# Performance work log

Hardware: AMD Instinct MI355X
Metric: run time of the kernel (lower is better)

## Reference

```python
import jax, jax.numpy as jnp
import numpy as np

DIM = 1024
HEADS = 16
NUM_EXPERTS = 8
TOP_K = 2
INNER = 4 * DIM
EPS = 1e-5
NEG = -1e9


def setup_inputs() -> dict:
    key = jax.random.key(0)
    ks = jax.random.split(key, 12)
    s = 0.02
    return {
        "x": jax.random.normal(ks[0], (4, 1024, DIM), dtype=jnp.float32),
        "qkv_w": jax.random.normal(ks[1], (DIM, 3 * DIM), dtype=jnp.float32) * s,
        "out_w": jax.random.normal(ks[2], (DIM, DIM), dtype=jnp.float32) * s,
        "out_b": jnp.zeros((DIM,), dtype=jnp.float32),
        "thresh": jnp.float32(-2.0),
        "ln1_g": jnp.ones((DIM,), dtype=jnp.float32),
        "ln1_b": jnp.zeros((DIM,), dtype=jnp.float32),
        "ln2_g": jnp.ones((DIM,), dtype=jnp.float32),
        "ln2_b": jnp.zeros((DIM,), dtype=jnp.float32),
        "gate_w": jax.random.normal(ks[3], (DIM, NUM_EXPERTS), dtype=jnp.float32) * s,
        "w1": jax.random.normal(ks[4], (NUM_EXPERTS, DIM, INNER), dtype=jnp.float32) * s,
        "b1": jnp.zeros((NUM_EXPERTS, INNER), dtype=jnp.float32),
        "w2": jax.random.normal(ks[5], (NUM_EXPERTS, INNER, DIM), dtype=jnp.float32) * s,
        "b2": jnp.zeros((NUM_EXPERTS, DIM), dtype=jnp.float32),
    }


def _layernorm(x, g, b):
    mu = jnp.mean(x, axis=-1, keepdims=True)
    var = jnp.mean(jnp.square(x - mu), axis=-1, keepdims=True)
    return (x - mu) * jax.lax.rsqrt(var + EPS) * g + b


def reference(x, qkv_w, out_w, out_b, thresh, ln1_g, ln1_b, ln2_g, ln2_b,
              gate_w, w1, b1, w2, b2):
    B, N, D = x.shape
    H = HEADS
    Dh = D // H
    scale = Dh ** -0.5

    # --- Sparse attention (pre-norm, eval mode: dropout off) ---
    h = _layernorm(x, ln1_g, ln1_b)
    qkv = h @ qkv_w                                   # [B,N,3D]
    q, k, v = jnp.split(qkv, 3, axis=-1)
    def heads(t):
        return t.reshape(B, N, H, Dh).transpose(0, 2, 1, 3)  # [B,H,N,Dh]
    q, k, v = heads(q), heads(k), heads(v)
    dots = jnp.einsum("bhid,bhjd->bhij", q, k) * scale
    dots = jnp.where(dots < thresh, jnp.float32(NEG), dots)  # learnable sparsity
    attn = jax.nn.softmax(dots, axis=-1)
    o = jnp.einsum("bhij,bhjd->bhid", attn, v)
    o = o.transpose(0, 2, 1, 3).reshape(B, N, D)
    x = x + o @ out_w + out_b

    # --- MoE FFN (pre-norm) ---
    h2 = _layernorm(x, ln2_g, ln2_b).reshape(-1, D)   # [T,D]
    T = h2.shape[0]
    logits = h2 @ gate_w                              # [T,E]
    probs = jax.nn.softmax(logits, axis=-1)
    aux_loss = NUM_EXPERTS * jnp.sum(probs.mean(0) * probs.sum(0))

    top_w, top_i = jax.lax.top_k(logits, TOP_K)       # [T,k]
    top_w = jax.nn.softmax(top_w, axis=-1)
    # dense combine weights: [T,E], zero for unselected experts
    combine = jnp.zeros((T, NUM_EXPERTS), dtype=h2.dtype)
    combine = combine.at[jnp.arange(T)[:, None], top_i].set(top_w)

    out = jnp.zeros_like(h2)
    for e in range(NUM_EXPERTS):
        y = jax.nn.gelu(h2 @ w1[e] + b1[e], approximate=False) @ w2[e] + b2[e]
        out = out + combine[:, e:e + 1] * y

    x = x + out.reshape(B, N, D)
    return x, aux_loss
```

## Files before the change

kernel.cpp:

```cpp
#include <hip/hip_runtime.h>
#include <math.h>

#define DIM 1024
#define THREE_DIM 3072
#define INNER 4096
#define NTOK 4096
#define NPAIR 8192
#define NEXP 8
#define MAXMB 72
#define PARTROWS (MAXMB*128)

typedef __attribute__((ext_vector_type(8))) short bf16x8;
typedef __attribute__((ext_vector_type(4))) float f32x4;

__device__ __forceinline__ unsigned short f2bf(float f){
    unsigned int x = __float_as_uint(f);
    unsigned int r = x + 0x7fffu + ((x >> 16) & 1u);
    return (unsigned short)(r >> 16);
}

__device__ __forceinline__ unsigned short us4c(ushort4 v, int i){
    return i == 0 ? v.x : (i == 1 ? v.y : (i == 2 ? v.z : v.w));
}

__device__ __forceinline__ void glds16(const void* g, void* l){
    __builtin_amdgcn_global_load_lds(
        (const __attribute__((address_space(1))) void*)g,
        (__attribute__((address_space(3))) void*)l, 16, 0, 0);
}

__device__ __forceinline__ int xcd_swz(){
    int cpx = gridDim.x >> 3;
    return (blockIdx.x & 7) * cpx + (blockIdx.x >> 3);
}

template<int WRITE_BF>
__global__ __launch_bounds__(256)
void ln_kernel(const float* __restrict__ X, const float* __restrict__ g,
               const float* __restrict__ b, float* __restrict__ outF,
               unsigned short* __restrict__ outB)
{
    int row = blockIdx.x;
    int t = threadIdx.x;
    const float4 v = *((const float4*)(X + (size_t)row*DIM) + t);
    float s = v.x + v.y + v.z + v.w;
    #pragma unroll
    for (int m = 1; m < 64; m <<= 1) s += __shfl_xor(s, m, 64);
    __shared__ float red[8];
    int wid = t >> 6, lane = t & 63;
    if (lane == 0) red[wid] = s;
    __syncthreads();
    float mu = (red[0]+red[1]+red[2]+red[3]) * (1.0f/DIM);
    float dx = v.x-mu, dy = v.y-mu, dz = v.z-mu, dw = v.w-mu;
    float s2 = dx*dx + dy*dy + dz*dz + dw*dw;
    #pragma unroll
    for (int m = 1; m < 64; m <<= 1) s2 += __shfl_xor(s2, m, 64);
    if (lane == 0) red[4+wid] = s2;
    __syncthreads();
    float var = (red[4]+red[5]+red[6]+red[7]) * (1.0f/DIM);
    float inv = rsqrtf(var + 1e-5f);
    const float4 gg = *((const float4*)g + t);
    const float4 bb = *((const float4*)b + t);
    float y0 = dx*inv*gg.x + bb.x;
    float y1 = dy*inv*gg.y + bb.y;
    float y2 = dz*inv*gg.z + bb.z;
    float y3 = dw*inv*gg.w + bb.w;
    if (outF){
        float4 o; o.x=y0; o.y=y1; o.z=y2; o.w=y3;
        *((float4*)(outF + (size_t)row*DIM) + t) = o;
    }
    if (WRITE_BF){
        ushort4 u; u.x=f2bf(y0); u.y=f2bf(y1); u.z=f2bf(y2); u.w=f2bf(y3);
        *((ushort4*)(outB + (size_t)row*DIM) + t) = u;
    }
}

template<int MODE>
__global__ __launch_bounds__(256)
void gemm_bf(const unsigned short* __restrict__ A,
             const unsigned short* __restrict__ BT,
             int K, int N, int gnx,
             const float* __restrict__ bias, const float* __restrict__ resid,
             unsigned short* __restrict__ outB, float* __restrict__ outF)
{
    __shared__ __align__(16) unsigned short As[128*64];
    __shared__ __align__(16) unsigned short Bs[128*64];
    int fid = xcd_swz();
    int nx = fid % gnx, my = fid / gnx;
    int m0 = my * 128, n0 = nx * 128;
    int t = threadIdx.x, lane = t & 63, wid = t >> 6;
    size_t aoff[4], boff[4];
    #pragma unroll
    for (int it = 0; it < 4; ++it){
        int chunk = it*256 + wid*64 + lane;
        int r = chunk >> 3, c16 = chunk & 7;
        int c16s = c16 ^ (r & 7);
        aoff[it] = (size_t)(m0 + r)*K + (size_t)(c16s*8);
        boff[it] = (size_t)(n0 + r)*K + (size_t)(c16s*8);
    }
    int wm = wid >> 1, wn = wid & 1;
    f32x4 acc[4][4];
    #pragma unroll
    for (int mi = 0; mi < 4; ++mi)
        #pragma unroll
        for (int ni = 0; ni < 4; ++ni)
            #pragma unroll
            for (int q = 0; q < 4; ++q) acc[mi][ni][q] = 0.f;

    for (int k0 = 0; k0 < K; k0 += 64){
        __syncthreads();
        #pragma unroll
        for (int it = 0; it < 4; ++it){
            glds16(A  + aoff[it] + k0, As + (size_t)(it*256 + wid*64)*8);
            glds16(BT + boff[it] + k0, Bs + (size_t)(it*256 + wid*64)*8);
        }
        __syncthreads();
        bf16x8 af[4][2], bg[4][2];
        #pragma unroll
        for (int mi = 0; mi < 4; ++mi){
            int row = wm*64 + mi*16 + (lane & 15);
            #pragma unroll
            for (int ks = 0; ks < 2; ++ks){
                int cg = (ks*4 + (lane >> 4)) ^ (row & 7);
                af[mi][ks] = *(const bf16x8*)&As[row*64 + cg*8];
            }
        }
        #pragma unroll
        for (int ni = 0; ni < 4; ++ni){
            int row = wn*64 + ni*16 + (lane & 15);
            #pragma unroll
            for (int ks = 0; ks < 2; ++ks){
                int cg = (ks*4 + (lane >> 4)) ^ (row & 7);
                bg[ni][ks] = *(const bf16x8*)&Bs[row*64 + cg*8];
            }
        }
        #pragma unroll
        for (int ks = 0; ks < 2; ++ks)
            #pragma unroll
            for (int mi = 0; mi < 4; ++mi)
                #pragma unroll
                for (int ni = 0; ni < 4; ++ni)
                    acc[mi][ni] = __builtin_amdgcn_mfma_f32_16x16x32_bf16(
                                      af[mi][ks], bg[ni][ks], acc[mi][ni], 0, 0, 0);
    }
    #pragma unroll
    for (int mi = 0; mi < 4; ++mi){
        #pragma unroll
        for (int ni = 0; ni < 4; ++ni){
            int ccol = n0 + wn*64 + ni*16 + (lane & 15);
            #pragma unroll
            for (int j = 0; j < 4; ++j){
                int row = m0 + wm*64 + mi*16 + (lane >> 4)*4 + j;
                float v = acc[mi][ni][j];
                if (MODE == 0){
                    outB[(size_t)row*N + ccol] = f2bf(v);
                } else {
                    outF[(size_t)row*N + ccol] =
                        v + bias[ccol] + resid[(size_t)row*N + ccol];
                }
            }
        }
    }
}

__global__ __launch_bounds__(256)
void attn4_kernel(const unsigned short* __restrict__ qkv,
                  unsigned short* __restrict__ O,
                  const float* __restrict__ threshp)
{
    __shared__ __align__(16) unsigned short Qs[64*64];
    __shared__ __align__(16) unsigned short Ks[64*64];
    __shared__ __align__(16) unsigned short Vp[8*520];
    __shared__ __align__(16) unsigned short Ps[4*1024];

    int fid = xcd_swz();
    int qt = fid & 15, hh = (fid >> 4) & 15, bb = fid >> 8;
    int t = threadIdx.x, lane = t & 63, w = t >> 6;
    int arow = lane & 15, agrp = lane >> 4;
    int qrow0 = bb*1024 + qt*64;
    float thresh = threshp[0];

    #pragma unroll
    for (int it = 0; it < 2; ++it){
        int chunk = it*256 + w*64 + lane;
        int r = chunk >> 3, c16 = chunk & 7;
        glds16(qkv + (size_t)(qrow0+r)*3072 + hh*64 + ((c16 ^ (r & 7))*8),
               Qs + (size_t)(it*256 + w*64)*8);
    }
    __syncthreads();
    bf16x8 qf[2];
    {
        int row = w*16 + arow;
        #pragma unroll
        for (int s = 0; s < 2; ++s){
            int c = (s*4 + agrp) ^ (row & 7);
            qf[s] = *(const bf16x8*)&Qs[row*64 + c*8];
        }
    }

    float m_[4], l_[4];
    f32x4 acc[4];
    #pragma unroll
    for (int j = 0; j < 4; ++j){ m_[j] = -INFINITY; l_[j] = 0.f; }
    #pragma unroll
    for (int d4 = 0; d4 < 4; ++d4)
        #pragma unroll
        for (int j = 0; j < 4; ++j) acc[d4][j] = 0.f;

    for (int kt = 0; kt < 16; ++kt){
        __syncthreads();
        int krow0 = bb*1024 + kt*64;
        #pragma unroll
        for (int it = 0; it < 2; ++it){
            int chunk = it*256 + w*64 + lane;
            int r = chunk >> 3, c16 = chunk & 7;
            glds16(qkv + (size_t)(krow0+r)*3072 + 1024 + hh*64 + ((c16 ^ (r & 7))*8),
                   Ks + (size_t)(it*256 + w*64)*8);
        }
        if (t < 128){
            int jc = t & 7, d0 = (t >> 3) * 4;
            ushort4 u[8];
            #pragma unroll
            for (int jj = 0; jj < 8; ++jj)
                u[jj] = *(const ushort4*)(qkv + (size_t)(krow0 + jc*8 + jj)*3072
                                          + 2048 + hh*64 + d0);
            #pragma unroll
            for (int i = 0; i < 4; ++i){
                ushort4 a, b;
                a.x = us4c(u[0], i); a.y = us4c(u[1], i);
                a.z = us4c(u[2], i); a.w = us4c(u[3], i);
                b.x = us4c(u[4], i); b.y = us4c(u[5], i);
                b.z = us4c(u[6], i); b.w = us4c(u[7], i);
                *(ushort4*)&Vp[jc*520 + (d0+i)*8]     = a;
                *(ushort4*)&Vp[jc*520 + (d0+i)*8 + 4] = b;
            }
        }
        __syncthreads();

        f32x4 sv[4];
        #pragma unroll
        for (int n = 0; n < 4; ++n)
            #pragma unroll
            for (int j = 0; j < 4; ++j) sv[n][j] = 0.f;
        #pragma unroll
        for (int n = 0; n < 4; ++n){
            int krow = n*16 + arow;
            #pragma unroll
            for (int s = 0; s < 2; ++s){
                int c = (s*4 + agrp) ^ (krow & 7);
                bf16x8 kf = *(const bf16x8*)&Ks[krow*64 + c*8];
                sv[n] = __builtin_amdgcn_mfma_f32_16x16x32_bf16(qf[s], kf, sv[n], 0, 0, 0);
            }
        }
        #pragma unroll
        for (int n = 0; n < 4; ++n)
            #pragma unroll
            for (int j = 0; j < 4; ++j){
                float s = sv[n][j] * 0.125f;
                sv[n][j] = (s < thresh) ? -1e9f : s;
            }
        float tmax[4], fac[4], rsum[4];
        #pragma unroll
        for (int j = 0; j < 4; ++j)
            tmax[j] = fmaxf(fmaxf(sv[0][j], sv[1][j]), fmaxf(sv[2][j], sv[3][j]));
        #pragma unroll
        for (int msk = 1; msk < 16; msk <<= 1)
            #pragma unroll
            for (int j = 0; j < 4; ++j)
                tmax[j] = fmaxf(tmax[j], __shfl_xor(tmax[j], msk, 64));
        #pragma unroll
        for (int j = 0; j < 4; ++j){
            float mn = fmaxf(m_[j], tmax[j]);
            fac[j] = __expf(m_[j] - mn);
            m_[j] = mn;
        }
        #pragma unroll
        for (int n = 0; n < 4; ++n)
            #pragma unroll
            for (int j = 0; j < 4; ++j)
                sv[n][j] = __expf(sv[n][j] - m_[j]);
        #pragma unroll
        for (int j = 0; j < 4; ++j)
            rsum[j] = sv[0][j] + sv[1][j] + sv[2][j] + sv[3][j];
        #pragma unroll
        for (int msk = 1; msk < 16; msk <<= 1)
            #pragma unroll
            for (int j = 0; j < 4; ++j)
                rsum[j] += __shfl_xor(rsum[j], msk, 64);
        #pragma unroll
        for (int j = 0; j < 4; ++j)
            l_[j] = l_[j]*fac[j] + rsum[j];
        #pragma unroll
        for (int n = 0; n < 4; ++n){
            int col = n*16 + arow;
            #pragma unroll
            for (int j = 0; j < 4; ++j){
                int r = agrp*4 + j;
                int idx = r*64 + (((col>>3) ^ (r&7)) << 3) + (col & 7);
                Ps[w*1024 + idx] = f2bf(sv[n][j]);
            }
        }
        #pragma unroll
        for (int d4 = 0; d4 < 4; ++d4)
            #pragma unroll
            for (int j = 0; j < 4; ++j) acc[d4][j] *= fac[j];
        #pragma unroll
        for (int s = 0; s < 2; ++s){
            int c = (s*4 + agrp) ^ (arow & 7);
            bf16x8 pa = *(const bf16x8*)&Ps[w*1024 + arow*64 + c*8];
            int jc = s*4 + agrp;
            #pragma unroll
            for (int d4 = 0; d4 < 4; ++d4){
                int dcol = d4*16 + arow;
                bf16x8 vb = *(const bf16x8*)&Vp[jc*520 + dcol*8];
                acc[d4] = __builtin_amdgcn_mfma_f32_16x16x32_bf16(pa, vb, acc[d4], 0, 0, 0);
            }
        }
    }
    #pragma unroll
    for (int j = 0; j < 4; ++j){
        float inv = 1.0f / l_[j];
        int row = qrow0 + w*16 + agrp*4 + j;
        #pragma unroll
        for (int d4 = 0; d4 < 4; ++d4)
            O[(size_t)row*1024 + hh*64 + d4*16 + arow] = f2bf(acc[d4][j] * inv);
    }
}

__global__ __launch_bounds__(64)
void gate_kernel(const float* __restrict__ h2, const float* __restrict__ gw,
                 float* __restrict__ probs, int* __restrict__ top_i,
                 float* __restrict__ top_w)
{
    int tk = blockIdx.x;
    int lane = threadIdx.x;
    const float* hr = h2 + (size_t)tk*DIM;
    float acc[8];
    #pragma unroll
    for (int e = 0; e < 8; ++e) acc[e] = 0.f;
    for (int d = lane; d < DIM; d += 64){
        float hv = hr[d];
        const float* grow = gw + d*8;
        #pragma unroll
        for (int e = 0; e < 8; ++e) acc[e] = fmaf(hv, grow[e], acc[e]);
    }
    #pragma unroll
    for (int m = 1; m < 64; m <<= 1)
        #pragma unroll
        for (int e = 0; e < 8; ++e) acc[e] += __shfl_xor(acc[e], m, 64);
    if (lane == 0){
        float mx = acc[0];
        #pragma unroll
        for (int e = 1; e < 8; ++e) mx = fmaxf(mx, acc[e]);
        float p[8], s = 0.f;
        #pragma unroll
        for (int e = 0; e < 8; ++e){ p[e] = __expf(acc[e]-mx); s += p[e]; }
        float invs = 1.f/s;
        #pragma unroll
        for (int e = 0; e < 8; ++e) probs[(size_t)tk*8+e] = p[e]*invs;
        int i0 = 0; float v0 = acc[0];
        #pragma unroll
        for (int e = 1; e < 8; ++e) if (acc[e] > v0){ v0 = acc[e]; i0 = e; }
        int i1 = -1; float v1 = -INFINITY;
        #pragma unroll
        for (int e = 0; e < 8; ++e) if (e != i0 && acc[e] > v1){ v1 = acc[e]; i1 = e; }
        float w0 = 1.f/(1.f + __expf(v1 - v0));
        top_i[tk*2]   = i0; top_i[tk*2+1] = i1;
        top_w[tk*2]   = w0; top_w[tk*2+1] = 1.f - w0;
    }
}

__global__ __launch_bounds__(256)
void aux_kernel(const float* __restrict__ probs, float* __restrict__ dout)
{
    int t = threadIdx.x;
    float acc[8];
    #pragma unroll
    for (int e = 0; e < 8; ++e) acc[e] = 0.f;
    for (int r = t; r < NTOK; r += 256){
        const float* pr = probs + (size_t)r*8;
        #pragma unroll
        for (int e = 0; e < 8; ++e) acc[e] += pr[e];
    }
    #pragma unroll
    for (int m = 1; m < 64; m <<= 1)
        #pragma unroll
        for (int e = 0; e < 8; ++e) acc[e] += __shfl_xor(acc[e], m, 64);
    __shared__ float red[4][8];
    int wid = t >> 6, lane = t & 63;
    if (lane == 0)
        for (int e = 0; e < 8; ++e) red[wid][e] = acc[e];
    __syncthreads();
    if (t == 0){
        float aux = 0.f;
        for (int e = 0; e < 8; ++e){
            float S = red[0][e]+red[1][e]+red[2][e]+red[3][e];
            aux += S*S;
        }
        dout[(size_t)NTOK*DIM] = aux * (8.0f/NTOK);
    }
}

__global__ __launch_bounds__(512)
void routing_kernel(const int* __restrict__ topi, int* __restrict__ perm,
                    int* __restrict__ mblk_e, int* __restrict__ tokslot)
{
    __shared__ int cnt[8];
    __shared__ int obase[8];
    int t = threadIdx.x, w = t >> 6, lane = t & 63;
    int c = 0;
    for (int i0 = 0; i0 < NPAIR; i0 += 64){
        int e = topi[i0 + lane];
        c += (e == w) ? 1 : 0;
    }
    #pragma unroll
    for (int m = 1; m < 64; m <<= 1) c += __shfl_xor(c, m, 64);
    if (lane == 0) cnt[w] = c;
    __syncthreads();
    if (t == 0){
        int mb = 0;
        for (int e = 0; e < 8; ++e){
            obase[e] = mb*128;
            int nb = (cnt[e] + 127) >> 7;
            for (int k = 0; k < nb; ++k) mblk_e[mb++] = e;
        }
        for (; mb < MAXMB; ++mb) mblk_e[mb] = -1;
    }
    __syncthreads();
    for (int i = t; i < MAXMB*128; i += 512) perm[i] = -1;
    __syncthreads();
    int base = obase[w];
    for (int i0 = 0; i0 < NPAIR; i0 += 64){
        int p = i0 + lane;
        int e = topi[p];
        bool mt = (e == w);
        unsigned long long mk = __ballot(mt);
        int rank = __popcll(mk & ((1ull << lane) - 1ull));
        if (mt){
            perm[base + rank] = p;
            tokslot[p] = base + rank;
        }
        base += __popcll(mk);
    }
}

template<int MODE>
__global__ __launch_bounds__(256)
void gemm_moe2(const unsigned short* __restrict__ Abase,
               const unsigned short* __restrict__ BTbase,
               int K, int N, int lda,
               const int* __restrict__ perm, const int* __restrict__ mblk_e,
               const float* __restrict__ bias,
               unsigned short* __restrict__ actout,
               float* __restrict__ partout)
{
    const int GNX = (MODE == 2) ? (INNER/128) : (DIM/128);
    int fid = xcd_swz();
    int nx = fid % GNX;
    int rest = fid / GNX;
    int mb = rest % MAXMB;
    int kk = rest / MAXMB;
    int e = mblk_e[mb];
    if (e < 0) return;
    int kspan = (MODE == 2) ? K : (K >> 1);
    int kbeg = kk * kspan, kend = kbeg + kspan;

    __shared__ __align__(16) unsigned short As[128*64];
    __shared__ __align__(16) unsigned short Bs[128*64];
    __shared__ int permL[128];
    int t = threadIdx.x;
    if (MODE == 2 && t < 128) permL[t] = perm[mb*128 + t];
    __syncthreads();
    int lane = t & 63, wid = t >> 6;
    int n0 = nx * 128;
    const unsigned short* BT = BTbase + (size_t)e * (size_t)N * (size_t)K;
    int base_chunk = wid*64 + lane;
    size_t aoff[4], boff[4];
    #pragma unroll
    for (int it = 0; it < 4; ++it){
        int chunk = base_chunk + it*256;
        int r = chunk >> 3, c16 = chunk & 7;
        int c16s = c16 ^ (r & 7);
        size_t ar;
        if (MODE == 2){ int p = permL[r]; ar = (p >= 0) ? (size_t)(p >> 1) : 0; }
        else          { ar = (size_t)(mb*128 + r); }
        aoff[it] = ar*(size_t)lda + (size_t)(c16s*8);
        boff[it] = (size_t)(n0 + r)*(size_t)K + (size_t)(c16s*8);
    }
    int wm = wid >> 1, wn = wid & 1;
    f32x4 acc[4][4];
    #pragma unroll
    for (int mi = 0; mi < 4; ++mi)
        #pragma unroll
        for (int ni = 0; ni < 4; ++ni)
            #pragma unroll
            for (int q = 0; q < 4; ++q) acc[mi][ni][q] = 0.f;

    for (int k0 = kbeg; k0 < kend; k0 += 64){
        __syncthreads();
        #pragma unroll
        for (int it = 0; it < 4; ++it){
            glds16(Abase + aoff[it] + k0, As + (size_t)(wid*64 + it*256)*8);
            glds16(BT    + boff[it] + k0, Bs + (size_t)(wid*64 + it*256)*8);
        }
        __syncthreads();
        bf16x8 af[4][2], bg[4][2];
        #pragma unroll
        for (int mi = 0; mi < 4; ++mi){
            int row = wm*64 + mi*16 + (lane & 15);
            #pragma unroll
            for (int ks = 0; ks < 2; ++ks){
                int cg = (ks*4 + (lane >> 4)) ^ (row & 7);
                af[mi][ks] = *(const bf16x8*)&As[row*64 + cg*8];
            }
        }
        #pragma unroll
        for (int ni = 0; ni < 4; ++ni){
            int row = wn*64 + ni*16 + (lane & 15);
            #pragma unroll
            for (int ks = 0; ks < 2; ++ks){
                int cg = (ks*4 + (lane >> 4)) ^ (row & 7);
                bg[ni][ks] = *(const bf16x8*)&Bs[row*64 + cg*8];
            }
        }
        #pragma unroll
        for (int ks = 0; ks < 2; ++ks)
            #pragma unroll
            for (int mi = 0; mi < 4; ++mi)
                #pragma unroll
                for (int ni = 0; ni < 4; ++ni)
                    acc[mi][ni] = __builtin_amdgcn_mfma_f32_16x16x32_bf16(
                                      af[mi][ks], bg[ni][ks], acc[mi][ni], 0, 0, 0);
    }
    #pragma unroll
    for (int mi = 0; mi < 4; ++mi){
        #pragma unroll
        for (int ni = 0; ni < 4; ++ni){
            int ccol = n0 + wn*64 + ni*16 + (lane & 15);
            float bv = (kk == 0) ? bias[(size_t)e*N + ccol] : 0.f;
            #pragma unroll
            for (int j = 0; j < 4; ++j){
                int rloc = wm*64 + mi*16 + (lane >> 4)*4 + j;
                float v = acc[mi][ni][j];
                if (MODE == 2){
                    float gx = v + bv;
                    float z2 = gx * fmaf(gx*gx, 0.07135481283f, 1.595769122f);
                    float ex = __expf(-z2);
                    float gl = gx * __builtin_amdgcn_rcpf(1.0f + ex);
                    actout[(size_t)(mb*128 + rloc)*N + ccol] = f2bf(gl);
                } else {
                    partout[((size_t)kk*PARTROWS + mb*128 + rloc)*N + ccol] = v + bv;
                }
            }
        }
    }
}

__global__ __launch_bounds__(256)
void combine_kernel(const float* __restrict__ part,
                    const int* __restrict__ tokslot,
                    const float* __restrict__ topw,
                    float* __restrict__ out)
{
    int tk = blockIdx.x, t = threadIdx.x;
    int s0 = tokslot[tk*2], s1 = tokslot[tk*2+1];
    float w0 = topw[tk*2], w1 = topw[tk*2+1];
    const float4* p00 = (const float4*)(part + (size_t)s0*DIM) + t;
    const float4* p10 = (const float4*)(part + ((size_t)PARTROWS + s0)*DIM) + t;
    const float4* p01 = (const float4*)(part + (size_t)s1*DIM) + t;
    const float4* p11 = (const float4*)(part + ((size_t)PARTROWS + s1)*DIM) + t;
    float4* o4 = (float4*)(out + (size_t)tk*DIM) + t;
    float4 a0 = *p00, a1 = *p10, b0 = *p01, b1 = *p11;
    float4 o = *o4;
    o.x += w0*(a0.x + a1.x) + w1*(b0.x + b1.x);
    o.y += w0*(a0.y + a1.y) + w1*(b0.y + b1.y);
    o.z += w0*(a0.z + a1.z) + w1*(b0.z + b1.z);
    o.w += w0*(a0.w + a1.w) + w1*(b0.w + b1.w);
    *o4 = o;
}

__global__ __launch_bounds__(256)
void transp_cast(const float* __restrict__ W, unsigned short* __restrict__ WT,
                 int K, int N)
{
    __shared__ float tile[32][33];
    size_t base = (size_t)blockIdx.z * (size_t)K * (size_t)N;
    const float* Wp = W + base;
    unsigned short* Tp = WT + base;
    int t = threadIdx.x;
    int r = t >> 3, c4 = (t & 7) << 2;
    int n0 = blockIdx.x << 5, k0 = blockIdx.y << 5;
    float4 v = *(const float4*)(Wp + (size_t)(k0+r)*N + n0 + c4);
    tile[r][c4+0] = v.x; tile[r][c4+1] = v.y;
    tile[r][c4+2] = v.z; tile[r][c4+3] = v.w;
    __syncthreads();
    ushort4 u;
    u.x = f2bf(tile[c4+0][r]);
    u.y = f2bf(tile[c4+1][r]);
    u.z = f2bf(tile[c4+2][r]);
    u.w = f2bf(tile[c4+3][r]);
    *(ushort4*)(Tp + (size_t)(n0+r)*K + k0 + c4) = u;
}

extern "C" void kernel_launch(void* const* d_in, const int* in_sizes, int n_in,
                              void* d_out, int out_size, void* d_ws, size_t ws_size,
                              hipStream_t stream)
{
    const float* x      = (const float*)d_in[0];
    const float* qkv_w  = (const float*)d_in[1];
    const float* out_w  = (const float*)d_in[2];
    const float* out_b  = (const float*)d_in[3];
    const float* thresh = (const float*)d_in[4];
    const float* ln1_g  = (const float*)d_in[5];
    const float* ln1_b  = (const float*)d_in[6];
    const float* ln2_g  = (const float*)d_in[7];
    const float* ln2_b  = (const float*)d_in[8];
    const float* gate_w = (const float*)d_in[9];
    const float* w1     = (const float*)d_in[10];
    const float* b1     = (const float*)d_in[11];
    const float* w2     = (const float*)d_in[12];
    const float* b2     = (const float*)d_in[13];
    float* out = (float*)d_out;
    char* ws = (char*)d_ws;

    const size_t MB = (size_t)1 << 20;
    unsigned short* h1bf  = (unsigned short*)(ws);
    unsigned short* qkvbf = (unsigned short*)(ws + 8*MB);
    unsigned short* obf   = (unsigned short*)(ws + 32*MB);
    float*          h2    = (float*)(ws + 40*MB);
    unsigned short* h2bf  = (unsigned short*)(ws + 56*MB);
    unsigned short* qwT   = (unsigned short*)(ws + 64*MB);
    unsigned short* owT   = (unsigned short*)(ws + 70*MB);
    unsigned short* w1T   = (unsigned short*)(ws + 72*MB);
    unsigned short* w2T   = (unsigned short*)(ws + 136*MB);
    unsigned short* act   = (unsigned short*)(ws + 200*MB);
    float* probs          = (float*)(ws + 276*MB);
    int*   top_i          = (int*)(ws + 276*MB + 131072);
    float* top_w          = (float*)(ws + 276*MB + 163840);
    int*   perm           = (int*)(ws + 276*MB + 196608);
    int*   mblk           = (int*)(ws + 276*MB + 237568);
    int*   tokslot        = (int*)(ws + 276*MB + 241664);
    float* part           = (float*)(ws + 280*MB);

    transp_cast<<<dim3(THREE_DIM/32, DIM/32, 1), 256, 0, stream>>>(qkv_w, qwT, DIM, THREE_DIM);
    transp_cast<<<dim3(DIM/32, DIM/32, 1), 256, 0, stream>>>(out_w, owT, DIM, DIM);

    ln_kernel<1><<<NTOK, 256, 0, stream>>>(x, ln1_g, ln1_b, nullptr, h1bf);
    gemm_bf<0><<<(THREE_DIM/128)*(NTOK/128), 256, 0, stream>>>(
        h1bf, qwT, DIM, THREE_DIM, THREE_DIM/128, nullptr, nullptr, qkvbf, nullptr);
    attn4_kernel<<<16*16*4, 256, 0, stream>>>(qkvbf, obf, thresh);
    gemm_bf<1><<<(DIM/128)*(NTOK/128), 256, 0, stream>>>(
        obf, owT, DIM, DIM, DIM/128, out_b, x, nullptr, out);
    ln_kernel<1><<<NTOK, 256, 0, stream>>>(out, ln2_g, ln2_b, h2, h2bf);
    gate_kernel<<<NTOK, 64, 0, stream>>>(h2, gate_w, probs, top_i, top_w);
    aux_kernel<<<1, 256, 0, stream>>>(probs, out);
    routing_kernel<<<1, 512, 0, stream>>>(top_i, perm, mblk, tokslot);

    transp_cast<<<dim3(INNER/32, DIM/32, NEXP), 256, 0, stream>>>(w1, w1T, DIM, INNER);
    transp_cast<<<dim3(DIM/32, INNER/32, NEXP), 256, 0, stream>>>(w2, w2T, INNER, DIM);

    gemm_moe2<2><<<(INNER/128)*MAXMB, 256, 0, stream>>>(
        h2bf, w1T, DIM, INNER, DIM, perm, mblk, b1, act, nullptr);
    gemm_moe2<3><<<(DIM/128)*MAXMB*2, 256, 0, stream>>>(
        act, w2T, INNER, DIM, INNER, perm, mblk, b2, nullptr, part);
    combine_kernel<<<NTOK, 256, 0, stream>>>(part, tokslot, top_w, out);
}
```

Before: 524.1 us.

## Double-buffer GEMM LDS tiles and store MoE partial sums in bf16

Both the dense GEMM and the MoE GEMM now use two LDS buffers, so the next K-tile is loaded asynchronously while MFMAs run on the current one. This replaces the two barriers per iteration with one. Separately, the split-K partial outputs of the second expert GEMM are stored as bf16 instead of fp32, which halves the partial-buffer write and read traffic in the combine kernel. The cost is doubled LDS per block, which may lower occupancy, plus extra rounding error in the partial sums.

```diff
diff --git a/kernel.cpp b/kernel.cpp
--- a/kernel.cpp
+++ b/kernel.cpp
@@ -17,6 +17,10 @@
     unsigned int x = __float_as_uint(f);
     unsigned int r = x + 0x7fffu + ((x >> 16) & 1u);
     return (unsigned short)(r >> 16);
+}
+
+__device__ __forceinline__ float bf2f(unsigned short u){
+    return __uint_as_float(((unsigned int)u) << 16);
 }
 
 __device__ __forceinline__ unsigned short us4c(ushort4 v, int i){
@@ -83,8 +87,8 @@
              const float* __restrict__ bias, const float* __restrict__ resid,
              unsigned short* __restrict__ outB, float* __restrict__ outF)
 {
-    __shared__ __align__(16) unsigned short As[128*64];
-    __shared__ __align__(16) unsigned short Bs[128*64];
+    __shared__ __align__(16) unsigned short As[2][128*64];
+    __shared__ __align__(16) unsigned short Bs[2][128*64];
     int fid = xcd_swz();
     int nx = fid % gnx, my = fid / gnx;
     int m0 = my * 128, n0 = nx * 128;
@@ -107,14 +111,24 @@
             #pragma unroll
             for (int q = 0; q < 4; ++q) acc[mi][ni][q] = 0.f;
 
+    #pragma unroll
+    for (int it = 0; it < 4; ++it){
+        glds16(A  + aoff[it], &As[0][(it*256 + wid*64)*8]);
+        glds16(BT + boff[it], &Bs[0][(it*256 + wid*64)*8]);
+    }
+    __syncthreads();
+    int cur = 0;
     for (int k0 = 0; k0 < K; k0 += 64){
-        __syncthreads();
-        #pragma unroll
-        for (int it = 0; it < 4; ++it){
-            glds16(A  + aoff[it] + k0, As + (size_t)(it*256 + wid*64)*8);
-            glds16(BT + boff[it] + k0, Bs + (size_t)(it*256 + wid*64)*8);
-        }
-        __syncthreads();
+        int knxt = k0 + 64;
+        if (knxt < K){
+            #pragma unroll
+            for (int it = 0; it < 4; ++it){
+                glds16(A  + aoff[it] + knxt, &As[cur^1][(it*256 + wid*64)*8]);
+                glds16(BT + boff[it] + knxt, &Bs[cur^1][(it*256 + wid*64)*8]);
+            }
+        }
+        const unsigned short* Asc = &As[cur][0];
+        const unsigned short* Bsc = &Bs[cur][0];
         bf16x8 af[4][2], bg[4][2];
         #pragma unroll
         for (int mi = 0; mi < 4; ++mi){
@@ -122,7 +136,7 @@
             #pragma unroll
             for (int ks = 0; ks < 2; ++ks){
                 int cg = (ks*4 + (lane >> 4)) ^ (row & 7);
-                af[mi][ks] = *(const bf16x8*)&As[row*64 + cg*8];
+                af[mi][ks] = *(const bf16x8*)&Asc[row*64 + cg*8];
             }
         }
         #pragma unroll
@@ -131,7 +145,7 @@
             #pragma unroll
             for (int ks = 0; ks < 2; ++ks){
                 int cg = (ks*4 + (lane >> 4)) ^ (row & 7);
-                bg[ni][ks] = *(const bf16x8*)&Bs[row*64 + cg*8];
+                bg[ni][ks] = *(const bf16x8*)&Bsc[row*64 + cg*8];
             }
         }
         #pragma unroll
@@ -142,6 +156,8 @@
                 for (int ni = 0; ni < 4; ++ni)
                     acc[mi][ni] = __builtin_amdgcn_mfma_f32_16x16x32_bf16(
                                       af[mi][ks], bg[ni][ks], acc[mi][ni], 0, 0, 0);
+        __syncthreads();
+        cur ^= 1;
     }
     #pragma unroll
     for (int mi = 0; mi < 4; ++mi){
@@ -452,7 +468,7 @@
                const int* __restrict__ perm, const int* __restrict__ mblk_e,
                const float* __restrict__ bias,
                unsigned short* __restrict__ actout,
-               float* __restrict__ partout)
+               unsigned short* __restrict__ partout)
 {
     const int GNX = (MODE == 2) ? (INNER/128) : (DIM/128);
     int fid = xcd_swz();
@@ -465,8 +481,8 @@
     int kspan = (MODE == 2) ? K : (K >> 1);
     int kbeg = kk * kspan, kend = kbeg + kspan;
 
-    __shared__ __align__(16) unsigned short As[128*64];
-    __shared__ __align__(16) unsigned short Bs[128*64];
+    __shared__ __align__(16) unsigned short As[2][128*64];
+    __shared__ __align__(16) unsigned short Bs[2][128*64];
     __shared__ int permL[128];
     int t = threadIdx.x;
     if (MODE == 2 && t < 128) permL[t] = perm[mb*128 + t];
@@ -496,14 +512,24 @@
             #pragma unroll
             for (int q = 0; q < 4; ++q) acc[mi][ni][q] = 0.f;
 
+    #pragma unroll
+    for (int it = 0; it < 4; ++it){
+        glds16(Abase + aoff[it] + kbeg, &As[0][(wid*64 + it*256)*8]);
+        glds16(BT    + boff[it] + kbeg, &Bs[0][(wid*64 + it*256)*8]);
+    }
+    __syncthreads();
+    int cur = 0;
     for (int k0 = kbeg; k0 < kend; k0 += 64){
-        __syncthreads();
-        #pragma unroll
-        for (int it = 0; it < 4; ++it){
-            glds16(Abase + aoff[it] + k0, As + (size_t)(wid*64 + it*256)*8);
-            glds16(BT    + boff[it] + k0, Bs + (size_t)(wid*64 + it*256)*8);
-        }
-        __syncthreads();
+        int knxt = k0 + 64;
+        if (knxt < kend){
+            #pragma unroll
+            for (int it = 0; it < 4; ++it){
+                glds16(Abase + aoff[it] + knxt, &As[cur^1][(wid*64 + it*256)*8]);
+                glds16(BT    + boff[it] + knxt, &Bs[cur^1][(wid*64 + it*256)*8]);
+            }
+        }
+        const unsigned short* Asc = &As[cur][0];
+        const unsigned short* Bsc = &Bs[cur][0];
         bf16x8 af[4][2], bg[4][2];
         #pragma unroll
         for (int mi = 0; mi < 4; ++mi){
@@ -511,7 +537,7 @@
             #pragma unroll
             for (int ks = 0; ks < 2; ++ks){
                 int cg = (ks*4 + (lane >> 4)) ^ (row & 7);
-                af[mi][ks] = *(const bf16x8*)&As[row*64 + cg*8];
+                af[mi][ks] = *(const bf16x8*)&Asc[row*64 + cg*8];
             }
         }
         #pragma unroll
@@ -520,7 +546,7 @@
             #pragma unroll
             for (int ks = 0; ks < 2; ++ks){
                 int cg = (ks*4 + (lane >> 4)) ^ (row & 7);
-                bg[ni][ks] = *(const bf16x8*)&Bs[row*64 + cg*8];
+                bg[ni][ks] = *(const bf16x8*)&Bsc[row*64 + cg*8];
             }
         }
         #pragma unroll
@@ -531,6 +557,8 @@
                 for (int ni = 0; ni < 4; ++ni)
                     acc[mi][ni] = __builtin_amdgcn_mfma_f32_16x16x32_bf16(
                                       af[mi][ks], bg[ni][ks], acc[mi][ni], 0, 0, 0);
+        __syncthreads();
+        cur ^= 1;
     }
     #pragma unroll
     for (int mi = 0; mi < 4; ++mi){
@@ -549,7 +577,7 @@
                     float gl = gx * __builtin_amdgcn_rcpf(1.0f + ex);
                     actout[(size_t)(mb*128 + rloc)*N + ccol] = f2bf(gl);
                 } else {
-                    partout[((size_t)kk*PARTROWS + mb*128 + rloc)*N + ccol] = v + bv;
+                    partout[((size_t)kk*PARTROWS + mb*128 + rloc)*N + ccol] = f2bf(v + bv);
                 }
             }
         }
@@ -557,7 +585,7 @@
 }
 
 __global__ __launch_bounds__(256)
-void combine_kernel(const float* __restrict__ part,
+void combine_kernel(const unsigned short* __restrict__ part,
                     const int* __restrict__ tokslot,
                     const float* __restrict__ topw,
                     float* __restrict__ out)
@@ -565,17 +593,16 @@
     int tk = blockIdx.x, t = threadIdx.x;
     int s0 = tokslot[tk*2], s1 = tokslot[tk*2+1];
     float w0 = topw[tk*2], w1 = topw[tk*2+1];
-    const float4* p00 = (const float4*)(part + (size_t)s0*DIM) + t;
-    const float4* p10 = (const float4*)(part + ((size_t)PARTROWS + s0)*DIM) + t;
-    const float4* p01 = (const float4*)(part + (size_t)s1*DIM) + t;
-    const float4* p11 = (const float4*)(part + ((size_t)PARTROWS + s1)*DIM) + t;
+    ushort4 a0 = *((const ushort4*)(part + (size_t)s0*DIM) + t);
+    ushort4 a1 = *((const ushort4*)(part + ((size_t)PARTROWS + s0)*DIM) + t);
+    ushort4 b0 = *((const ushort4*)(part + (size_t)s1*DIM) + t);
+    ushort4 b1 = *((const ushort4*)(part + ((size_t)PARTROWS + s1)*DIM) + t);
     float4* o4 = (float4*)(out + (size_t)tk*DIM) + t;
-    float4 a0 = *p00, a1 = *p10, b0 = *p01, b1 = *p11;
     float4 o = *o4;
-    o.x += w0*(a0.x + a1.x) + w1*(b0.x + b1.x);
-    o.y += w0*(a0.y + a1.y) + w1*(b0.y + b1.y);
-    o.z += w0*(a0.z + a1.z) + w1*(b0.z + b1.z);
-    o.w += w0*(a0.w + a1.w) + w1*(b0.w + b1.w);
+    o.x += w0*(bf2f(a0.x) + bf2f(a1.x)) + w1*(bf2f(b0.x) + bf2f(b1.x));
+    o.y += w0*(bf2f(a0.y) + bf2f(a1.y)) + w1*(bf2f(b0.y) + bf2f(b1.y));
+    o.z += w0*(bf2f(a0.z) + bf2f(a1.z)) + w1*(bf2f(b0.z) + bf2f(b1.z));
+    o.w += w0*(bf2f(a0.w) + bf2f(a1.w)) + w1*(bf2f(b0.w) + bf2f(b1.w));
     *o4 = o;
 }
 
@@ -640,7 +667,7 @@
     int*   perm           = (int*)(ws + 276*MB + 196608);
     int*   mblk           = (int*)(ws + 276*MB + 237568);
     int*   tokslot        = (int*)(ws + 276*MB + 241664);
-    float* part           = (float*)(ws + 280*MB);
+    unsigned short* part  = (unsigned short*)(ws + 280*MB);
 
     transp_cast<<<dim3(THREE_DIM/32, DIM/32, 1), 256, 0, stream>>>(qkv_w, qwT, DIM, THREE_DIM);
     transp_cast<<<dim3(DIM/32, DIM/32, 1), 256, 0, stream>>>(out_w, owT, DIM, DIM);
```

After: 567.9 us. 1.08x slower.

## Widen MoE GEMM tiles to 128x256 with 512 threads and store partials as bf16

Applied to the files above, without the earlier changes.

The MoE expert GEMMs now use 128x256 output tiles computed by 8 waves of 512 threads, so each A tile loaded into shared memory is reused across twice as many output columns. The fragment loads are restructured per k-substep to cut register pressure. The split-K partial outputs of the second GEMM are stored as bf16 instead of fp32, which halves the partial-buffer write and read traffic in combine_kernel. The trade-offs are fewer blocks, which may lower occupancy and load balance, and reduced precision in the summed partials.

```diff
diff --git a/kernel.cpp b/kernel.cpp
--- a/kernel.cpp
+++ b/kernel.cpp
@@ -17,6 +17,10 @@
     unsigned int x = __float_as_uint(f);
     unsigned int r = x + 0x7fffu + ((x >> 16) & 1u);
     return (unsigned short)(r >> 16);
+}
+
+__device__ __forceinline__ float bf2f(unsigned short u){
+    return __uint_as_float(((unsigned int)u) << 16);
 }
 
 __device__ __forceinline__ unsigned short us4c(ushort4 v, int i){
@@ -445,16 +449,16 @@
 }
 
 template<int MODE>
-__global__ __launch_bounds__(256)
-void gemm_moe2(const unsigned short* __restrict__ Abase,
+__global__ __launch_bounds__(512, 4)
+void gemm_moe3(const unsigned short* __restrict__ Abase,
                const unsigned short* __restrict__ BTbase,
                int K, int N, int lda,
                const int* __restrict__ perm, const int* __restrict__ mblk_e,
                const float* __restrict__ bias,
                unsigned short* __restrict__ actout,
-               float* __restrict__ partout)
-{
-    const int GNX = (MODE == 2) ? (INNER/128) : (DIM/128);
+               unsigned short* __restrict__ partout)
+{
+    const int GNX = (MODE == 2) ? (INNER/256) : (DIM/256);
     int fid = xcd_swz();
     int nx = fid % GNX;
     int rest = fid / GNX;
@@ -466,28 +470,33 @@
     int kbeg = kk * kspan, kend = kbeg + kspan;
 
     __shared__ __align__(16) unsigned short As[128*64];
-    __shared__ __align__(16) unsigned short Bs[128*64];
+    __shared__ __align__(16) unsigned short Bs[256*64];
     __shared__ int permL[128];
     int t = threadIdx.x;
     if (MODE == 2 && t < 128) permL[t] = perm[mb*128 + t];
     __syncthreads();
     int lane = t & 63, wid = t >> 6;
-    int n0 = nx * 128;
+    int wm = wid >> 2, wn = wid & 3;
+    int n0 = nx * 256;
     const unsigned short* BT = BTbase + (size_t)e * (size_t)N * (size_t)K;
-    int base_chunk = wid*64 + lane;
-    size_t aoff[4], boff[4];
-    #pragma unroll
-    for (int it = 0; it < 4; ++it){
-        int chunk = base_chunk + it*256;
+    size_t aoff[2], boff[4];
+    #pragma unroll
+    for (int it = 0; it < 2; ++it){
+        int chunk = it*512 + t;
         int r = chunk >> 3, c16 = chunk & 7;
         int c16s = c16 ^ (r & 7);
         size_t ar;
         if (MODE == 2){ int p = permL[r]; ar = (p >= 0) ? (size_t)(p >> 1) : 0; }
         else          { ar = (size_t)(mb*128 + r); }
         aoff[it] = ar*(size_t)lda + (size_t)(c16s*8);
+    }
+    #pragma unroll
+    for (int it = 0; it < 4; ++it){
+        int chunk = it*512 + t;
+        int r = chunk >> 3, c16 = chunk & 7;
+        int c16s = c16 ^ (r & 7);
         boff[it] = (size_t)(n0 + r)*(size_t)K + (size_t)(c16s*8);
     }
-    int wm = wid >> 1, wn = wid & 1;
     f32x4 acc[4][4];
     #pragma unroll
     for (int mi = 0; mi < 4; ++mi)
@@ -499,38 +508,34 @@
     for (int k0 = kbeg; k0 < kend; k0 += 64){
         __syncthreads();
         #pragma unroll
-        for (int it = 0; it < 4; ++it){
-            glds16(Abase + aoff[it] + k0, As + (size_t)(wid*64 + it*256)*8);
-            glds16(BT    + boff[it] + k0, Bs + (size_t)(wid*64 + it*256)*8);
-        }
+        for (int it = 0; it < 2; ++it)
+            glds16(Abase + aoff[it] + k0, As + (size_t)(it*512 + wid*64)*8);
+        #pragma unroll
+        for (int it = 0; it < 4; ++it)
+            glds16(BT    + boff[it] + k0, Bs + (size_t)(it*512 + wid*64)*8);
         __syncthreads();
-        bf16x8 af[4][2], bg[4][2];
-        #pragma unroll
-        for (int mi = 0; mi < 4; ++mi){
-            int row = wm*64 + mi*16 + (lane & 15);
-            #pragma unroll
-            for (int ks = 0; ks < 2; ++ks){
+        #pragma unroll
+        for (int ks = 0; ks < 2; ++ks){
+            bf16x8 af[4], bg[4];
+            #pragma unroll
+            for (int mi = 0; mi < 4; ++mi){
+                int row = wm*64 + mi*16 + (lane & 15);
                 int cg = (ks*4 + (lane >> 4)) ^ (row & 7);
-                af[mi][ks] = *(const bf16x8*)&As[row*64 + cg*8];
-            }
-        }
-        #pragma unroll
-        for (int ni = 0; ni < 4; ++ni){
-            int row = wn*64 + ni*16 + (lane & 15);
-            #pragma unroll
-            for (int ks = 0; ks < 2; ++ks){
+                af[mi] = *(const bf16x8*)&As[row*64 + cg*8];
+            }
+            #pragma unroll
+            for (int ni = 0; ni < 4; ++ni){
+                int row = wn*64 + ni*16 + (lane & 15);
                 int cg = (ks*4 + (lane >> 4)) ^ (row & 7);
-                bg[ni][ks] = *(const bf16x8*)&Bs[row*64 + cg*8];
-            }
-        }
-        #pragma unroll
-        for (int ks = 0; ks < 2; ++ks)
+                bg[ni] = *(const bf16x8*)&Bs[row*64 + cg*8];
+            }
             #pragma unroll
             for (int mi = 0; mi < 4; ++mi)
                 #pragma unroll
                 for (int ni = 0; ni < 4; ++ni)
                     acc[mi][ni] = __builtin_amdgcn_mfma_f32_16x16x32_bf16(
-                                      af[mi][ks], bg[ni][ks], acc[mi][ni], 0, 0, 0);
+                                      af[mi], bg[ni], acc[mi][ni], 0, 0, 0);
+        }
     }
     #pragma unroll
     for (int mi = 0; mi < 4; ++mi){
@@ -549,7 +554,7 @@
                     float gl = gx * __builtin_amdgcn_rcpf(1.0f + ex);
                     actout[(size_t)(mb*128 + rloc)*N + ccol] = f2bf(gl);
                 } else {
-                    partout[((size_t)kk*PARTROWS + mb*128 + rloc)*N + ccol] = v + bv;
+                    partout[((size_t)kk*PARTROWS + mb*128 + rloc)*N + ccol] = f2bf(v + bv);
                 }
             }
         }
@@ -557,7 +562,7 @@
 }
 
 __global__ __launch_bounds__(256)
-void combine_kernel(const float* __restrict__ part,
+void combine_kernel(const unsigned short* __restrict__ part,
                     const int* __restrict__ tokslot,
                     const float* __restrict__ topw,
                     float* __restrict__ out)
@@ -565,17 +570,16 @@
     int tk = blockIdx.x, t = threadIdx.x;
     int s0 = tokslot[tk*2], s1 = tokslot[tk*2+1];
     float w0 = topw[tk*2], w1 = topw[tk*2+1];
-    const float4* p00 = (const float4*)(part + (size_t)s0*DIM) + t;
-    const float4* p10 = (const float4*)(part + ((size_t)PARTROWS + s0)*DIM) + t;
-    const float4* p01 = (const float4*)(part + (size_t)s1*DIM) + t;
-    const float4* p11 = (const float4*)(part + ((size_t)PARTROWS + s1)*DIM) + t;
+    ushort4 a0 = *((const ushort4*)(part + (size_t)s0*DIM) + t);
+    ushort4 a1 = *((const ushort4*)(part + ((size_t)PARTROWS + s0)*DIM) + t);
+    ushort4 b0 = *((const ushort4*)(part + (size_t)s1*DIM) + t);
+    ushort4 b1 = *((const ushort4*)(part + ((size_t)PARTROWS + s1)*DIM) + t);
     float4* o4 = (float4*)(out + (size_t)tk*DIM) + t;
-    float4 a0 = *p00, a1 = *p10, b0 = *p01, b1 = *p11;
     float4 o = *o4;
-    o.x += w0*(a0.x + a1.x) + w1*(b0.x + b1.x);
-    o.y += w0*(a0.y + a1.y) + w1*(b0.y + b1.y);
-    o.z += w0*(a0.z + a1.z) + w1*(b0.z + b1.z);
-    o.w += w0*(a0.w + a1.w) + w1*(b0.w + b1.w);
+    o.x += w0*(bf2f(a0.x) + bf2f(a1.x)) + w1*(bf2f(b0.x) + bf2f(b1.x));
+    o.y += w0*(bf2f(a0.y) + bf2f(a1.y)) + w1*(bf2f(b0.y) + bf2f(b1.y));
+    o.z += w0*(bf2f(a0.z) + bf2f(a1.z)) + w1*(bf2f(b0.z) + bf2f(b1.z));
+    o.w += w0*(bf2f(a0.w) + bf2f(a1.w)) + w1*(bf2f(b0.w) + bf2f(b1.w));
     *o4 = o;
 }
 
@@ -640,7 +644,7 @@
     int*   perm           = (int*)(ws + 276*MB + 196608);
     int*   mblk           = (int*)(ws + 276*MB + 237568);
     int*   tokslot        = (int*)(ws + 276*MB + 241664);
-    float* part           = (float*)(ws + 280*MB);
+    unsigned short* part  = (unsigned short*)(ws + 280*MB);
 
     transp_cast<<<dim3(THREE_DIM/32, DIM/32, 1), 256, 0, stream>>>(qkv_w, qwT, DIM, THREE_DIM);
     transp_cast<<<dim3(DIM/32, DIM/32, 1), 256, 0, stream>>>(out_w, owT, DIM, DIM);
@@ -659,9 +663,9 @@
     transp_cast<<<dim3(INNER/32, DIM/32, NEXP), 256, 0, stream>>>(w1, w1T, DIM, INNER);
     transp_cast<<<dim3(DIM/32, INNER/32, NEXP), 256, 0, stream>>>(w2, w2T, INNER, DIM);
 
-    gemm_moe2<2><<<(INNER/128)*MAXMB, 256, 0, stream>>>(
+    gemm_moe3<2><<<(INNER/256)*MAXMB, 512, 0, stream>>>(
         h2bf, w1T, DIM, INNER, DIM, perm, mblk, b1, act, nullptr);
-    gemm_moe2<3><<<(DIM/128)*MAXMB*2, 256, 0, stream>>>(
+    gemm_moe3<3><<<(DIM/256)*MAXMB*2, 512, 0, stream>>>(
         act, w2T, INNER, DIM, INNER, perm, mblk, b2, nullptr, part);
     combine_kernel<<<NTOK, 256, 0, stream>>>(part, tokslot, top_w, out);
 }
```

Result: faster. 510.1 us (-2.7%).
